# Optimization experiments

Hardware: AMD Instinct MI355X
Metric: run time of the kernel (lower is better)

The kernel has to match this reference:

```python
import jax, jax.numpy as jnp
import numpy as np
import itertools


def setup_inputs() -> dict:
    key = jax.random.key(0)
    k1, k2 = jax.random.split(key)
    B, D, H, W, C = 2, 160, 160, 160, 2
    vol = jax.random.normal(k1, (B, D, H, W, C), dtype=jnp.float32)
    # dense displacement field, a few voxels of motion (typical registration flow)
    trf = jax.random.normal(k2, (B, D, H, W, 3), dtype=jnp.float32) * 3.0
    return {"vol": vol, "trf": trf}


def _interp_single(vol, shift):
    """vol: [D,H,W,C], shift: [D,H,W,3] -> warped [D,H,W,C].
    Faithful to transform()+interpn(interp_method='linear', indexing='ij')."""
    volshape = vol.shape[:-1]
    nd = len(volshape)  # 3
    # mesh + shift = absolute sample locations (float)
    mesh = jnp.meshgrid(*[jnp.arange(d, dtype=jnp.float32) for d in volshape],
                        indexing='ij')
    loc = jnp.stack(mesh, axis=-1) + shift  # [D,H,W,3]

    loc0 = jnp.floor(loc)
    max_loc = jnp.array([d - 1 for d in volshape], dtype=jnp.float32)  # [3]
    loc0c = jnp.clip(loc0, 0.0, max_loc)          # clipped floor corner
    loc1c = jnp.clip(loc0c + 1.0, 0.0, max_loc)   # clipped ceil corner

    # NOTE: weights use clipped loc1 vs UNclipped loc, exactly as the TF code
    d1 = loc1c - loc        # weight paired with corner bit 0 (floor)
    d0 = 1.0 - d1           # weight paired with corner bit 1 (ceil)
    locs = (loc0c.astype(jnp.int32), loc1c.astype(jnp.int32))
    wts = (d1, d0)

    out = jnp.zeros(volshape + (vol.shape[-1],), dtype=vol.dtype)
    # 2^3 = 8 corner gathers + weighted accumulation (same as sub2ind + tf.gather)
    for c in itertools.product([0, 1], repeat=nd):
        idx = tuple(locs[c[d]][..., d] for d in range(nd))
        w = wts[c[0]][..., 0] * wts[c[1]][..., 1] * wts[c[2]][..., 2]
        out = out + w[..., None] * vol[idx]
    return out


def reference(vol, trf):
    # single_transform=False: per-sample warp (tf.map_fn over batch)
    return jax.vmap(_interp_single)(vol, trf)
```

## Files before the change

### kernel.cpp

```cpp
#include <hip/hip_runtime.h>


#define BLK 256
constexpr int Bn = 2, Dn = 160, Hn = 160, Wn = 160;
constexpr int HQ = 40;
constexpr int RSTRIP = HQ * Wn;
constexpr int HQ2 = 20;
constexpr int RSTRIP2 = HQ2 * Wn;
constexpr int V = 4;

typedef float    f32x2  __attribute__((ext_vector_type(2)));
typedef float    f32x4  __attribute__((ext_vector_type(4), aligned(8)));
typedef _Float16 h16x8  __attribute__((ext_vector_type(8), aligned(8)));
typedef _Float16 h16x16 __attribute__((ext_vector_type(16), aligned(16)));

__global__ __launch_bounds__(BLK) void repack_dh(
    const float* __restrict__ vol, _Float16* __restrict__ pk)
{
    const int t  = blockIdx.x * BLK + threadIdx.x;
    const int v0 = t * 2;
    const int w  = v0 % Wn;
    const int r  = v0 / Wn;
    const int h  = r % Hn;
    const int d  = (r / Hn) % Dn;
    const int dh = (h < Hn - 1) ? 1 : 0;
    const int dd = (d < Dn - 1) ? Hn : 0;

    const int r00 = r;
    const int r01 = r + dh;
    const int r10 = r + dd;
    const int r11 = r + dd + dh;

    const f32x4 A = *(const f32x4*)(vol + ((long long)(r00 * Wn + w) << 1));
    const f32x4 B = *(const f32x4*)(vol + ((long long)(r01 * Wn + w) << 1));
    const f32x4 C = *(const f32x4*)(vol + ((long long)(r10 * Wn + w) << 1));
    const f32x4 D = *(const f32x4*)(vol + ((long long)(r11 * Wn + w) << 1));

    h16x16 o;
    o[0]  = (_Float16)A.x; o[1]  = (_Float16)A.y;
    o[2]  = (_Float16)B.x; o[3]  = (_Float16)B.y;
    o[4]  = (_Float16)C.x; o[5]  = (_Float16)C.y;
    o[6]  = (_Float16)D.x; o[7]  = (_Float16)D.y;
    o[8]  = (_Float16)A.z; o[9]  = (_Float16)A.w;
    o[10] = (_Float16)B.z; o[11] = (_Float16)B.w;
    o[12] = (_Float16)C.z; o[13] = (_Float16)C.w;
    o[14] = (_Float16)D.z; o[15] = (_Float16)D.w;
    *(h16x16*)(pk + ((long long)v0 << 3)) = o;
}

__global__ __launch_bounds__(BLK, 4) void st_warp_kernel_pk16(
    const _Float16* __restrict__ pk,
    const float* __restrict__ trf,
    float* __restrict__ out,
    const int b)
{
    const int tid = threadIdx.x;
    const int sl  = blockIdx.x & 7;
    const int j   = blockIdx.x >> 3;
    const int h0  = sl * HQ2;

    int   gvox[V], dk[V], hk[V], wk[V];
    float sd[V], sh[V], sw[V];
    #pragma unroll
    for (int k = 0; k < V; ++k) {
        const int v   = j * (BLK * V) + k * BLK + tid;
        const int d   = v / RSTRIP2;
        const int rem = v - d * RSTRIP2;
        const int hh  = rem / Wn;
        const int w   = rem - hh * Wn;
        dk[k] = d; hk[k] = h0 + hh; wk[k] = w;
        gvox[k] = ((b * Dn + d) * Hn + (h0 + hh)) * Wn + w;
    }
    #pragma unroll
    for (int k = 0; k < V; ++k) {
        const float* tp = trf + (long long)gvox[k] * 3;
        sd[k] = __builtin_nontemporal_load(tp + 0);
        sh[k] = __builtin_nontemporal_load(tp + 1);
        sw[k] = __builtin_nontemporal_load(tp + 2);
    }
    __builtin_amdgcn_sched_barrier(0);

    h16x16 val[V];
    float wA[V], wB[V], wC[V], wD[V], w0[V], w1[V];
    #pragma unroll
    for (int k = 0; k < V; ++k) {
        float loc, c0f, c1f;

        loc = (float)dk[k] + sd[k];
        c0f = fminf(fmaxf(floorf(loc), 0.0f), (float)(Dn - 1));
        c1f = fminf(c0f + 1.0f, (float)(Dn - 1));
        const float wd0 = c1f - loc, wd1 = 1.0f - wd0;
        const int id0 = (int)c0f;

        loc = (float)hk[k] + sh[k];
        c0f = fminf(fmaxf(floorf(loc), 0.0f), (float)(Hn - 1));
        c1f = fminf(c0f + 1.0f, (float)(Hn - 1));
        const float wh0 = c1f - loc, wh1 = 1.0f - wh0;
        const int ih0 = (int)c0f;

        loc = (float)wk[k] + sw[k];
        c0f = fminf(fmaxf(floorf(loc), 0.0f), (float)(Wn - 1));
        c1f = fminf(c0f + 1.0f, (float)(Wn - 1));
        const float ww0 = c1f - loc, ww1 = 1.0f - ww0;
        const int iw0 = (int)c0f;

        const bool lo = (iw0 < Wn - 1);
        const int  m  = lo ? iw0 : (Wn - 2);
        w0[k] = lo ? ww0 : 0.0f;
        w1[k] = lo ? ww1 : 1.0f;
        wA[k] = wd0 * wh0; wB[k] = wd0 * wh1;
        wC[k] = wd1 * wh0; wD[k] = wd1 * wh1;

        const long long p0 = ((b * Dn + id0) * Hn + ih0) * Wn + m;
        val[k] = *(const h16x16*)(pk + (p0 << 3));
    }
    __builtin_amdgcn_sched_barrier(0);

    #pragma unroll
    for (int k = 0; k < V; ++k) {
        const h16x16 v = val[k];
        const float acc0 =
              wA[k] * (w0[k] * (float)v[0] + w1[k] * (float)v[8])
            + wB[k] * (w0[k] * (float)v[2] + w1[k] * (float)v[10])
            + wC[k] * (w0[k] * (float)v[4] + w1[k] * (float)v[12])
            + wD[k] * (w0[k] * (float)v[6] + w1[k] * (float)v[14]);
        const float acc1 =
              wA[k] * (w0[k] * (float)v[1] + w1[k] * (float)v[9])
            + wB[k] * (w0[k] * (float)v[3] + w1[k] * (float)v[11])
            + wC[k] * (w0[k] * (float)v[5] + w1[k] * (float)v[13])
            + wD[k] * (w0[k] * (float)v[7] + w1[k] * (float)v[15]);
        f32x2 res; res.x = acc0; res.y = acc1;
        __builtin_nontemporal_store(res, &((f32x2*)out)[gvox[k]]);
    }
}

__global__ __launch_bounds__(BLK) void repack_h_pairs(
    const float* __restrict__ vol, _Float16* __restrict__ pk)
{
    const int t  = blockIdx.x * BLK + threadIdx.x;
    const int v0 = t * 2;
    const int w  = v0 % Wn;
    const int r  = v0 / Wn;
    const int h  = r % Hn;
    const int hc = (h < Hn - 1) ? (h + 1) : h;
    const int r1 = r - h + hc;

    const f32x4 a = *(const f32x4*)(vol + ((long long)v0 << 1));
    const f32x4 b = *(const f32x4*)(vol + ((long long)(r1 * Wn + w) << 1));

    h16x8 o;
    o[0] = (_Float16)a.x; o[1] = (_Float16)a.y;
    o[2] = (_Float16)b.x; o[3] = (_Float16)b.y;
    o[4] = (_Float16)a.z; o[5] = (_Float16)a.w;
    o[6] = (_Float16)b.z; o[7] = (_Float16)b.w;
    *(h16x8*)(pk + ((long long)v0 << 2)) = o;
}

__global__ __launch_bounds__(BLK, 4) void st_warp_kernel_pk(
    const _Float16* __restrict__ pk,
    const float* __restrict__ trf,
    float* __restrict__ out)
{
    const int tid = threadIdx.x;
    const int xcd = blockIdx.x & 7;
    const int j   = blockIdx.x >> 3;
    const int b   = xcd >> 2;
    const int h0  = (xcd & 3) * HQ;

    int   gvox[V];
    float sd[V], sh[V], sw[V];
    #pragma unroll
    for (int k = 0; k < V; ++k) {
        const int v   = j * (BLK * V) + k * BLK + tid;
        const int d   = v / RSTRIP;
        const int rem = v - d * RSTRIP;
        const int hh  = rem / Wn;
        const int w   = rem - hh * Wn;
        gvox[k] = ((b * Dn + d) * Hn + (h0 + hh)) * Wn + w;
    }
    #pragma unroll
    for (int k = 0; k < V; ++k) {
        const float* tp = trf + (long long)gvox[k] * 3;
        sd[k] = __builtin_nontemporal_load(tp + 0);
        sh[k] = __builtin_nontemporal_load(tp + 1);
        sw[k] = __builtin_nontemporal_load(tp + 2);
    }

    h16x8 val[2 * V];
    float wA[V], wB[V], wC[V], wD[V], w0[V], w1[V];
    #pragma unroll
    for (int k = 0; k < V; ++k) {
        const int v   = j * (BLK * V) + k * BLK + tid;
        const int d   = v / RSTRIP;
        const int rem = v - d * RSTRIP;
        const int hh  = rem / Wn;
        const int w   = rem - hh * Wn;
        const int h   = h0 + hh;

        float loc, c0f, c1f;

        loc = (float)d + sd[k];
        c0f = fminf(fmaxf(floorf(loc), 0.0f), (float)(Dn - 1));
        c1f = fminf(c0f + 1.0f, (float)(Dn - 1));
        const float wd0 = c1f - loc, wd1 = 1.0f - wd0;
        const int id0 = (int)c0f, id1 = (int)c1f;

        loc = (float)h + sh[k];
        c0f = fminf(fmaxf(floorf(loc), 0.0f), (float)(Hn - 1));
        c1f = fminf(c0f + 1.0f, (float)(Hn - 1));
        const float wh0 = c1f - loc, wh1 = 1.0f - wh0;
        const int ih0 = (int)c0f;

        loc = (float)w + sw[k];
        c0f = fminf(fmaxf(floorf(loc), 0.0f), (float)(Wn - 1));
        c1f = fminf(c0f + 1.0f, (float)(Wn - 1));
        const float ww0 = c1f - loc, ww1 = 1.0f - ww0;
        const int iw0 = (int)c0f;

        const bool lo = (iw0 < Wn - 1);
        const int  m  = lo ? iw0 : (Wn - 2);
        w0[k] = lo ? ww0 : 0.0f;
        w1[k] = lo ? ww1 : 1.0f;
        wA[k] = wd0 * wh0; wB[k] = wd0 * wh1;
        wC[k] = wd1 * wh0; wD[k] = wd1 * wh1;

        const int bo = b * Dn;
        const int p0 = ((bo + id0) * Hn + ih0) * Wn + m;
        const int p1 = ((bo + id1) * Hn + ih0) * Wn + m;

        val[2 * k + 0] = *(const h16x8*)(pk + ((long long)p0 << 2));
        val[2 * k + 1] = *(const h16x8*)(pk + ((long long)p1 << 2));
    }

    #pragma unroll
    for (int k = 0; k < V; ++k) {
        const h16x8 a = val[2 * k + 0];
        const h16x8 c = val[2 * k + 1];
        const float acc0 =
              wA[k] * (w0[k] * (float)a[0] + w1[k] * (float)a[4])
            + wB[k] * (w0[k] * (float)a[2] + w1[k] * (float)a[6])
            + wC[k] * (w0[k] * (float)c[0] + w1[k] * (float)c[4])
            + wD[k] * (w0[k] * (float)c[2] + w1[k] * (float)c[6]);
        const float acc1 =
              wA[k] * (w0[k] * (float)a[1] + w1[k] * (float)a[5])
            + wB[k] * (w0[k] * (float)a[3] + w1[k] * (float)a[7])
            + wC[k] * (w0[k] * (float)c[1] + w1[k] * (float)c[5])
            + wD[k] * (w0[k] * (float)c[3] + w1[k] * (float)c[7]);
        f32x2 res; res.x = acc0; res.y = acc1;
        __builtin_nontemporal_store(res, &((f32x2*)out)[gvox[k]]);
    }
}

__global__ __launch_bounds__(BLK, 4) void st_warp_kernel_f32(
    const float* __restrict__ vol,
    const float* __restrict__ trf,
    float* __restrict__ out)
{
    const int tid = threadIdx.x;
    const int xcd = blockIdx.x & 7;
    const int j   = blockIdx.x >> 3;
    const int b   = xcd >> 2;
    const int h0  = (xcd & 3) * HQ;

    int   gvox[V];
    float sd[V], sh[V], sw[V];
    #pragma unroll
    for (int k = 0; k < V; ++k) {
        const int v   = j * (BLK * V) + k * BLK + tid;
        const int d   = v / RSTRIP;
        const int rem = v - d * RSTRIP;
        const int hh  = rem / Wn;
        const int w   = rem - hh * Wn;
        gvox[k] = ((b * Dn + d) * Hn + (h0 + hh)) * Wn + w;
    }
    #pragma unroll
    for (int k = 0; k < V; ++k) {
        const float* tp = trf + (long long)gvox[k] * 3;
        sd[k] = __builtin_nontemporal_load(tp + 0);
        sh[k] = __builtin_nontemporal_load(tp + 1);
        sw[k] = __builtin_nontemporal_load(tp + 2);
    }

    f32x4 val[4 * V];
    float wA[V], wB[V], wC[V], wD[V], w0[V], w1[V];
    #pragma unroll
    for (int k = 0; k < V; ++k) {
        const int v   = j * (BLK * V) + k * BLK + tid;
        const int d   = v / RSTRIP;
        const int rem = v - d * RSTRIP;
        const int hh  = rem / Wn;
        const int w   = rem - hh * Wn;
        const int h   = h0 + hh;

        float loc, c0f, c1f;

        loc = (float)d + sd[k];
        c0f = fminf(fmaxf(floorf(loc), 0.0f), (float)(Dn - 1));
        c1f = fminf(c0f + 1.0f, (float)(Dn - 1));
        const float wd0 = c1f - loc, wd1 = 1.0f - wd0;
        const int id0 = (int)c0f, id1 = (int)c1f;

        loc = (float)h + sh[k];
        c0f = fminf(fmaxf(floorf(loc), 0.0f), (float)(Hn - 1));
        c1f = fminf(c0f + 1.0f, (float)(Hn - 1));
        const float wh0 = c1f - loc, wh1 = 1.0f - wh0;
        const int ih0 = (int)c0f, ih1 = (int)c1f;

        loc = (float)w + sw[k];
        c0f = fminf(fmaxf(floorf(loc), 0.0f), (float)(Wn - 1));
        c1f = fminf(c0f + 1.0f, (float)(Wn - 1));
        const float ww0 = c1f - loc, ww1 = 1.0f - ww0;
        const int iw0 = (int)c0f;

        const bool lo = (iw0 < Wn - 1);
        const int  m  = lo ? iw0 : (Wn - 2);
        w0[k] = lo ? ww0 : 0.0f;
        w1[k] = lo ? ww1 : 1.0f;
        wA[k] = wd0 * wh0; wB[k] = wd0 * wh1;
        wC[k] = wd1 * wh0; wD[k] = wd1 * wh1;

        const int bo  = b * Dn;
        const int r00 = ((bo + id0) * Hn + ih0) * Wn;
        const int r01 = ((bo + id0) * Hn + ih1) * Wn;
        const int r10 = ((bo + id1) * Hn + ih0) * Wn;
        const int r11 = ((bo + id1) * Hn + ih1) * Wn;

        val[4 * k + 0] = *(const f32x4*)(vol + (((long long)(r00 + m)) << 1));
        val[4 * k + 1] = *(const f32x4*)(vol + (((long long)(r01 + m)) << 1));
        val[4 * k + 2] = *(const f32x4*)(vol + (((long long)(r10 + m)) << 1));
        val[4 * k + 3] = *(const f32x4*)(vol + (((long long)(r11 + m)) << 1));
    }

    #pragma unroll
    for (int k = 0; k < V; ++k) {
        const f32x4 vA = val[4 * k + 0], vB = val[4 * k + 1];
        const f32x4 vC = val[4 * k + 2], vD = val[4 * k + 3];
        const float acc0 = wA[k] * (w0[k] * vA.x + w1[k] * vA.z)
                         + wB[k] * (w0[k] * vB.x + w1[k] * vB.z)
                         + wC[k] * (w0[k] * vC.x + w1[k] * vC.z)
                         + wD[k] * (w0[k] * vD.x + w1[k] * vD.z);
        const float acc1 = wA[k] * (w0[k] * vA.y + w1[k] * vA.w)
                         + wB[k] * (w0[k] * vB.y + w1[k] * vB.w)
                         + wC[k] * (w0[k] * vC.y + w1[k] * vC.w)
                         + wD[k] * (w0[k] * vD.y + w1[k] * vD.w);
        f32x2 res; res.x = acc0; res.y = acc1;
        __builtin_nontemporal_store(res, &((f32x2*)out)[gvox[k]]);
    }
}

extern "C" void kernel_launch(void* const* d_in, const int* in_sizes, int n_in,
                              void* d_out, int out_size, void* d_ws, size_t ws_size,
                              hipStream_t stream) {
    const float* vol = (const float*)d_in[0];
    const float* trf = (const float*)d_in[1];
    float* out = (float*)d_out;

    const int nvox = Bn * Dn * Hn * Wn;
    const size_t pk16_bytes = (size_t)nvox * 8 * sizeof(_Float16);
    const size_t pk8_bytes  = (size_t)nvox * 4 * sizeof(_Float16);
    const int rgrid = (nvox / 2) / BLK;

    if (d_ws != nullptr && ws_size >= pk16_bytes) {
        _Float16* pk = (_Float16*)d_ws;
        const int hgrid = (nvox / 2) / (BLK * V);
        repack_dh<<<rgrid, BLK, 0, stream>>>(vol, pk);
        st_warp_kernel_pk16<<<hgrid, BLK, 0, stream>>>(pk, trf, out, 0);
        st_warp_kernel_pk16<<<hgrid, BLK, 0, stream>>>(pk, trf, out, 1);
    } else if (d_ws != nullptr && ws_size >= pk8_bytes) {
        _Float16* pk = (_Float16*)d_ws;
        const int grid = nvox / (BLK * V);
        repack_h_pairs<<<rgrid, BLK, 0, stream>>>(vol, pk);
        st_warp_kernel_pk<<<grid, BLK, 0, stream>>>(pk, trf, out);
    } else {
        const int grid = nvox / (BLK * V);
        st_warp_kernel_f32<<<grid, BLK, 0, stream>>>(vol, trf, out);
    }
}
```

Measured before the change: 276.7 us.

## Split each voxel's 32-byte gather across a lane pair with shuffle reduction

Each output voxel is now handled by two adjacent lanes. Each lane loads one 16-byte half of the packed fp16 corner record (the w or w+1 column), computes a partial weighted sum, and the pair combines the halves with __shfl_xor; only the even lane stores. The aim is smaller per-lane gathers and more lanes in flight per voxel to hide gather latency. In exchange the index and trf-load work is duplicated across both lanes, the grid doubles, and half the lanes sit idle during the store.

```diff
diff --git a/kernel.cpp b/kernel.cpp
--- a/kernel.cpp
+++ b/kernel.cpp
@@ -12,6 +12,7 @@
 typedef float    f32x2  __attribute__((ext_vector_type(2)));
 typedef float    f32x4  __attribute__((ext_vector_type(4), aligned(8)));
 typedef _Float16 h16x8  __attribute__((ext_vector_type(8), aligned(8)));
+typedef _Float16 h16x8a __attribute__((ext_vector_type(8), aligned(16)));
 typedef _Float16 h16x16 __attribute__((ext_vector_type(16), aligned(16)));
 
 __global__ __launch_bounds__(BLK) void repack_dh(
@@ -48,22 +49,24 @@
     *(h16x16*)(pk + ((long long)v0 << 3)) = o;
 }
 
-__global__ __launch_bounds__(BLK, 4) void st_warp_kernel_pk16(
+__global__ __launch_bounds__(BLK, 4) void st_warp_kernel_pair(
     const _Float16* __restrict__ pk,
     const float* __restrict__ trf,
     float* __restrict__ out,
     const int b)
 {
-    const int tid = threadIdx.x;
-    const int sl  = blockIdx.x & 7;
-    const int j   = blockIdx.x >> 3;
-    const int h0  = sl * HQ2;
+    const int tid  = threadIdx.x;
+    const int i    = tid >> 1;
+    const int half = tid & 1;
+    const int sl   = blockIdx.x & 7;
+    const int j    = blockIdx.x >> 3;
+    const int h0   = sl * HQ2;
 
     int   gvox[V], dk[V], hk[V], wk[V];
     float sd[V], sh[V], sw[V];
     #pragma unroll
     for (int k = 0; k < V; ++k) {
-        const int v   = j * (BLK * V) + k * BLK + tid;
+        const int v   = j * ((BLK / 2) * V) + k * (BLK / 2) + i;
         const int d   = v / RSTRIP2;
         const int rem = v - d * RSTRIP2;
         const int hh  = rem / Wn;
@@ -80,8 +83,8 @@
     }
     __builtin_amdgcn_sched_barrier(0);
 
-    h16x16 val[V];
-    float wA[V], wB[V], wC[V], wD[V], w0[V], w1[V];
+    h16x8a val[V];
+    float wA[V], wB[V], wC[V], wD[V], wsel[V];
     #pragma unroll
     for (int k = 0; k < V; ++k) {
         float loc, c0f, c1f;
@@ -106,31 +109,32 @@
 
         const bool lo = (iw0 < Wn - 1);
         const int  m  = lo ? iw0 : (Wn - 2);
-        w0[k] = lo ? ww0 : 0.0f;
-        w1[k] = lo ? ww1 : 1.0f;
+        const float w0 = lo ? ww0 : 0.0f;
+        const float w1 = lo ? ww1 : 1.0f;
+        wsel[k] = half ? w1 : w0;
         wA[k] = wd0 * wh0; wB[k] = wd0 * wh1;
         wC[k] = wd1 * wh0; wD[k] = wd1 * wh1;
 
-        const long long p0 = ((b * Dn + id0) * Hn + ih0) * Wn + m;
-        val[k] = *(const h16x16*)(pk + (p0 << 3));
+        const long long p = ((b * Dn + id0) * Hn + ih0) * Wn + m + half;
+        val[k] = *(const h16x8a*)(pk + (p << 3));
     }
     __builtin_amdgcn_sched_barrier(0);
 
     #pragma unroll
     for (int k = 0; k < V; ++k) {
-        const h16x16 v = val[k];
-        const float acc0 =
-              wA[k] * (w0[k] * (float)v[0] + w1[k] * (float)v[8])
-            + wB[k] * (w0[k] * (float)v[2] + w1[k] * (float)v[10])
-            + wC[k] * (w0[k] * (float)v[4] + w1[k] * (float)v[12])
-            + wD[k] * (w0[k] * (float)v[6] + w1[k] * (float)v[14]);
-        const float acc1 =
-              wA[k] * (w0[k] * (float)v[1] + w1[k] * (float)v[9])
-            + wB[k] * (w0[k] * (float)v[3] + w1[k] * (float)v[11])
-            + wC[k] * (w0[k] * (float)v[5] + w1[k] * (float)v[13])
-            + wD[k] * (w0[k] * (float)v[7] + w1[k] * (float)v[15]);
-        f32x2 res; res.x = acc0; res.y = acc1;
-        __builtin_nontemporal_store(res, &((f32x2*)out)[gvox[k]]);
+        const h16x8a v = val[k];
+        const float part0 = wsel[k] *
+              (wA[k] * (float)v[0] + wB[k] * (float)v[2]
+             + wC[k] * (float)v[4] + wD[k] * (float)v[6]);
+        const float part1 = wsel[k] *
+              (wA[k] * (float)v[1] + wB[k] * (float)v[3]
+             + wC[k] * (float)v[5] + wD[k] * (float)v[7]);
+        const float acc0 = part0 + __shfl_xor(part0, 1);
+        const float acc1 = part1 + __shfl_xor(part1, 1);
+        if (half == 0) {
+            f32x2 res; res.x = acc0; res.y = acc1;
+            __builtin_nontemporal_store(res, &((f32x2*)out)[gvox[k]]);
+        }
     }
 }
 
@@ -362,10 +366,10 @@
 
     if (d_ws != nullptr && ws_size >= pk16_bytes) {
         _Float16* pk = (_Float16*)d_ws;
-        const int hgrid = (nvox / 2) / (BLK * V);
+        const int hgrid = (nvox / 2) / ((BLK / 2) * V);
         repack_dh<<<rgrid, BLK, 0, stream>>>(vol, pk);
-        st_warp_kernel_pk16<<<hgrid, BLK, 0, stream>>>(pk, trf, out, 0);
-        st_warp_kernel_pk16<<<hgrid, BLK, 0, stream>>>(pk, trf, out, 1);
+        st_warp_kernel_pair<<<hgrid, BLK, 0, stream>>>(pk, trf, out, 0);
+        st_warp_kernel_pair<<<hgrid, BLK, 0, stream>>>(pk, trf, out, 1);
     } else if (d_ws != nullptr && ws_size >= pk8_bytes) {
         _Float16* pk = (_Float16*)d_ws;
         const int grid = nvox / (BLK * V);
```

Measured after the change: 279.7 us. About the same (+1.1%).
